# Performance work log

Hardware: AMD Instinct MI355X
Metric: run time of the kernel (lower is better)

The kernel has to match this reference:

```python
import jax, jax.numpy as jnp
from jax import lax
import numpy as np

D_MODEL, D_STATE, D_CONV, EXPAND = 512, 16, 4, 2
D_INNER = EXPAND * D_MODEL
B_SZ, SEQ = 16, 2048


def setup_inputs() -> dict:
    key = jax.random.key(0)
    ks = jax.random.split(key, 8)
    s = 0.02
    x = jax.random.normal(ks[0], (B_SZ, SEQ, D_MODEL), jnp.float32)
    W_in = jax.random.normal(ks[1], (2 * D_INNER, D_MODEL), jnp.float32) * s
    conv_w = jax.random.normal(ks[2], (D_INNER, 1, D_CONV), jnp.float32) * s
    conv_b = jnp.zeros((D_INNER,), jnp.float32)
    W_x = jax.random.normal(ks[3], (2 * D_STATE, D_INNER), jnp.float32) * s
    W_dt = jax.random.normal(ks[4], (D_INNER, D_INNER), jnp.float32) * s
    b_dt = jnp.zeros((D_INNER,), jnp.float32)
    # A_log = -logspace(log10(0.001), log10(1.0), d_state), exactly as in source
    A_log = jnp.asarray(-np.logspace(np.log10(0.001), 0.0, D_STATE), jnp.float32)
    D = jnp.ones((D_INNER,), jnp.float32) * 0.1
    W_out = jax.random.normal(ks[5], (D_MODEL, D_INNER), jnp.float32) * s
    ln_g = jnp.ones((D_MODEL,), jnp.float32)
    ln_b = jnp.zeros((D_MODEL,), jnp.float32)
    return dict(x=x, W_in=W_in, conv_w=conv_w, conv_b=conv_b, W_x=W_x,
                W_dt=W_dt, b_dt=b_dt, A_log=A_log, D=D, W_out=W_out,
                ln_g=ln_g, ln_b=ln_b)


def _selective_scan(u, delta, A, B, C, Dp):
    # u, delta: [b, s, di]; B, C: [b, s, ds]; A: [ds]; Dp: [di]
    def step(state, inp):
        d_t, u_t, B_t, C_t = inp            # [b,di],[b,di],[b,ds],[b,ds]
        dA = jnp.exp(jnp.clip(d_t[:, :, None] * A[None, None, :], -5.0, 5.0))
        dBu = (d_t * u_t)[:, :, None] * B_t[:, None, :]
        state = dA * state + dBu            # [b,di,ds]
        y_t = jnp.einsum('bds,bs->bd', state, C_t)
        return state, y_t

    b = u.shape[0]
    init = jnp.zeros((b, D_INNER, D_STATE), u.dtype)
    xs = (delta.transpose(1, 0, 2), u.transpose(1, 0, 2),
          B.transpose(1, 0, 2), C.transpose(1, 0, 2))
    _, ys = lax.scan(step, init, xs)        # [s, b, di]
    return ys.transpose(1, 0, 2) + u * Dp


def reference(x, W_in, conv_w, conv_b, W_x, W_dt, b_dt, A_log, D, W_out, ln_g, ln_b):
    x = jnp.clip(x, -10.0, 10.0)
    x_and_res = x @ W_in.T                  # [b, s, 2*di]
    x_p, res = jnp.split(x_and_res, 2, axis=-1)
    # causal depthwise conv1d (left pad d_conv-1, truncate to seq_len)
    xc = lax.conv_general_dilated(
        x_p.transpose(0, 2, 1), conv_w, window_strides=(1,),
        padding=[(D_CONV - 1, 0)], dimension_numbers=('NCH', 'OIH', 'NCH'),
        feature_group_count=D_INNER)
    xc = (xc + conv_b[None, :, None]).transpose(0, 2, 1)  # [b, s, di]
    xc = jax.nn.silu(xc)
    ssm = xc @ W_x.T                        # [b, s, 2*ds]
    Bm, Cm = jnp.split(ssm, 2, axis=-1)
    dt = xc @ W_dt.T + b_dt                 # [b, s, di]
    y = _selective_scan(xc, dt, A_log, Bm, Cm, D)
    y = y * jax.nn.silu(res)
    out = y @ W_out.T + x
    # LayerNorm (eps=1e-5)
    mu = out.mean(-1, keepdims=True)
    var = ((out - mu) ** 2).mean(-1, keepdims=True)
    return (out - mu) * lax.rsqrt(var + 1e-5) * ln_g + ln_b
```

## Files before the change

### kernel.cpp

```cpp
#include <hip/hip_runtime.h>
#include <hip/hip_bf16.h>
#include <math.h>

#define B_SZ 16
#define SEQ 2048
#define D_MODEL 512
#define D_INNER 1024
#define D_STATE 16
#define D_CONV 4
#define NSEG 32
#define SEGLEN (SEQ / NSEG)
#define GRP (SEGLEN / 4)
#define LOG2E 1.44269504f

typedef __attribute__((ext_vector_type(8))) short short8;
typedef __attribute__((ext_vector_type(4))) float f32x4;
typedef const __attribute__((address_space(1))) void* gas_ptr;
typedef __attribute__((address_space(3))) void* las_ptr;

__device__ __forceinline__ float bf2f(unsigned int bits16) {
    union { unsigned int i; float f; } v; v.i = bits16 << 16; return v.f;
}
__device__ __forceinline__ unsigned short f2bf(float f) {
    union { float f; unsigned int i; } v; v.f = f;
    unsigned int r = v.i + 0x7FFFu + ((v.i >> 16) & 1u);
    return (unsigned short)(r >> 16);
}
__device__ __forceinline__ void async_g2l(const void* g, void* l) {
    __builtin_amdgcn_global_load_lds((gas_ptr)g, (las_ptr)l, 16, 0, 0);
}
__device__ __forceinline__ float fast_exp2(float x) { return __builtin_amdgcn_exp2f(x); }
__device__ __forceinline__ float fast_rcp(float x)  { return __builtin_amdgcn_rcpf(x); }
__device__ __forceinline__ float clamp3(float x, float lo, float hi) {
    return __builtin_amdgcn_fmed3f(x, lo, hi);
}
__device__ __forceinline__ float silu(float x) {
    return x * fast_rcp(1.f + fast_exp2(-x * LOG2E));
}
__device__ __forceinline__ void vm_wait0() { asm volatile("s_waitcnt vmcnt(0)" ::: "memory"); }
__device__ __forceinline__ void vm_wait3() { asm volatile("s_waitcnt vmcnt(3)" ::: "memory"); }
__device__ __forceinline__ void vm_wait4() { asm volatile("s_waitcnt vmcnt(4)" ::: "memory"); }

__global__ __launch_bounds__(256) void cast_bf16(
    const float4* __restrict__ in, ushort4* __restrict__ out, int n4, int do_clip)
{
    int i = blockIdx.x * 256 + threadIdx.x;
    if (i >= n4) return;
    float4 v = in[i];
    if (do_clip) {
        v.x = clamp3(v.x, -10.f, 10.f);
        v.y = clamp3(v.y, -10.f, 10.f);
        v.z = clamp3(v.z, -10.f, 10.f);
        v.w = clamp3(v.w, -10.f, 10.f);
    }
    ushort4 o;
    o.x = f2bf(v.x); o.y = f2bf(v.y); o.z = f2bf(v.z); o.w = f2bf(v.w);
    out[i] = o;
}

__global__ __launch_bounds__(256) void cast5(
    const float4* __restrict__ W_in, const float4* __restrict__ W_dt,
    const float4* __restrict__ W_out, const float4* __restrict__ W_x,
    const float4* __restrict__ x,
    ushort4* __restrict__ Wib, ushort4* __restrict__ Wdtb,
    ushort4* __restrict__ Wob, ushort4* __restrict__ Wxb,
    ushort4* __restrict__ xbf, int n4x)
{
    const int A0 = 262144;
    const int A1 = A0 + 262144;
    const int A2 = A1 + 131072;
    const int A3 = A2 + 8192;
    int i = blockIdx.x * 256 + threadIdx.x;
    const float4* src; ushort4* dst; int j; int clip = 0;
    if (i < A0)      { src = W_in;  dst = Wib;  j = i; }
    else if (i < A1) { src = W_dt;  dst = Wdtb; j = i - A0; }
    else if (i < A2) { src = W_out; dst = Wob;  j = i - A1; }
    else if (i < A3) { src = W_x;   dst = Wxb;  j = i - A2; }
    else             { j = i - A3; if (j >= n4x) return; src = x; dst = xbf; clip = 1; }
    float4 v = src[j];
    if (clip) {
        v.x = clamp3(v.x, -10.f, 10.f);
        v.y = clamp3(v.y, -10.f, 10.f);
        v.z = clamp3(v.z, -10.f, 10.f);
        v.w = clamp3(v.w, -10.f, 10.f);
    }
    ushort4 o;
    o.x = f2bf(v.x); o.y = f2bf(v.y); o.z = f2bf(v.z); o.w = f2bf(v.w);
    dst[j] = o;
}

__global__ __launch_bounds__(512, 4) void gemm_big(
    const unsigned short* __restrict__ A, const unsigned short* __restrict__ Bw,
    void* __restrict__ C, int K, int ldc, int nbn_shift,
    const float* __restrict__ bias,
    const float* __restrict__ add, int ldadd, int clip_add, int out_bf16)
{
    __shared__ unsigned short As[3][256][32];
    __shared__ unsigned short Bs[3][128][32];
    const int h = blockIdx.x;
    const int xk = h & 7;
    const int qb = h >> 3;
    const int bn = (qb & ((1 << nbn_shift) - 1)) * 128;
    const int bm = ((qb >> nbn_shift) * 8 + xk) * 256;
    const int tid = threadIdx.x;
    const int wv = tid >> 6;
    const int l  = tid & 63;
    const int lr = l >> 2;
    const int lc = l & 3;
    const int wm = (wv >> 1) * 64;
    const int wn = (wv & 1) * 64;
    const int r16 = l & 15;
    const int q   = l >> 4;
    const int gsw = (lc - ((lr >> 1) & 3)) & 3;
    const int ssw = ((q + ((r16 >> 1) & 3)) & 3) * 8;

    f32x4 acc[4][4];
    #pragma unroll
    for (int i = 0; i < 4; i++)
        #pragma unroll
        for (int j = 0; j < 4; j++)
            acc[i][j] = (f32x4){0.f, 0.f, 0.f, 0.f};

#define STAGEB(kk, bb) { \
        const int k0_ = (kk) * 32; \
        _Pragma("unroll") \
        for (int p_ = 0; p_ < 2; p_++) { \
            const int arow_ = wv * 32 + p_ * 16 + lr; \
            async_g2l((const char*)A + (((size_t)(bm + arow_)) * K + k0_ + gsw * 8) * 2, \
                      (char*)&As[bb][wv * 32 + p_ * 16][0]); \
        } \
        const int brow_ = wv * 16 + lr; \
        async_g2l((const char*)Bw + (((size_t)(bn + brow_)) * K + k0_ + gsw * 8) * 2, \
                  (char*)&Bs[bb][wv * 16][0]); \
    }

    const int nk = K >> 5;
    STAGEB(0, 0);
    STAGEB(1, 1);
    int c0 = 0, c1 = 1, c2 = 2;

    for (int kk = 0; kk < nk; kk++) {
        if (kk + 1 < nk) vm_wait3(); else vm_wait0();
        __builtin_amdgcn_s_barrier();

        short8 af[4], bfv[4];
        #pragma unroll
        for (int i = 0; i < 4; i++) {
            af[i]  = *(const short8*)&As[c0][wm + i * 16 + r16][ssw];
            bfv[i] = *(const short8*)&Bs[c0][wn + i * 16 + r16][ssw];
        }
        if (kk + 2 < nk) STAGEB(kk + 2, c2);

        #pragma unroll
        for (int i = 0; i < 4; i++)
            #pragma unroll
            for (int j = 0; j < 4; j++)
                acc[i][j] = __builtin_amdgcn_mfma_f32_16x16x32_bf16(
                    af[i], bfv[j], acc[i][j], 0, 0, 0);

        int t = c0; c0 = c1; c1 = c2; c2 = t;
    }
#undef STAGEB

    #pragma unroll
    for (int i = 0; i < 4; i++) {
        #pragma unroll
        for (int rr = 0; rr < 4; rr++) {
            int m = bm + wm + i * 16 + q * 4 + rr;
            #pragma unroll
            for (int j = 0; j < 4; j++) {
                int n = bn + wn + j * 16 + r16;
                float v = acc[i][j][rr];
                if (bias) v += bias[n];
                if (add) {
                    float a = add[(size_t)m * ldadd + n];
                    if (clip_add) a = clamp3(a, -10.f, 10.f);
                    v += a;
                }
                if (out_bf16)
                    ((unsigned short*)C)[(size_t)m * ldc + n] = f2bf(v);
                else
                    ((float*)C)[(size_t)m * ldc + n] = v;
            }
        }
    }
}

__global__ __launch_bounds__(256) void gemm_bf16(
    const unsigned short* __restrict__ A, const unsigned short* __restrict__ Bw,
    void* __restrict__ C, int K, int ldc, int nbn_shift,
    const float* __restrict__ bias,
    const float* __restrict__ add, int ldadd, int clip_add, int out_bf16)
{
    __shared__ unsigned short As[3][128][32];
    __shared__ unsigned short Bs[3][128][32];
    const int h = blockIdx.x;
    const int xk = h & 7;
    const int qb = h >> 3;
    const int bn = (qb & ((1 << nbn_shift) - 1)) * 128;
    const int bm = ((qb >> nbn_shift) * 8 + xk) * 128;
    const int tid = threadIdx.x;
    const int wv = tid >> 6;
    const int l  = tid & 63;
    const int lr = l >> 2;
    const int lc = l & 3;
    const int wm = (wv >> 1) * 64;
    const int wn = (wv & 1) * 64;
    const int r16 = l & 15;
    const int q   = l >> 4;
    const int gsw = (lc - ((lr >> 1) & 3)) & 3;
    const int ssw = ((q + ((r16 >> 1) & 3)) & 3) * 8;

    f32x4 acc[4][4];
    #pragma unroll
    for (int i = 0; i < 4; i++)
        #pragma unroll
        for (int j = 0; j < 4; j++)
            acc[i][j] = (f32x4){0.f, 0.f, 0.f, 0.f};

#define STAGE(kk, bb) { \
        const int k0_ = (kk) * 32; \
        _Pragma("unroll") \
        for (int p_ = 0; p_ < 2; p_++) { \
            const int row_ = wv * 32 + p_ * 16 + lr; \
            async_g2l((const char*)A + (((size_t)(bm + row_)) * K + k0_ + gsw * 8) * 2, \
                      (char*)&As[bb][wv * 32 + p_ * 16][0]); \
            async_g2l((const char*)Bw + (((size_t)(bn + row_)) * K + k0_ + gsw * 8) * 2, \
                      (char*)&Bs[bb][wv * 32 + p_ * 16][0]); \
        } }

    const int nk = K >> 5;
    STAGE(0, 0);
    STAGE(1, 1);
    int c0 = 0, c1 = 1, c2 = 2;

    for (int kk = 0; kk < nk; kk++) {
        if (kk + 1 < nk) vm_wait4(); else vm_wait0();
        __builtin_amdgcn_s_barrier();

        short8 af[4], bfv[4];
        #pragma unroll
        for (int i = 0; i < 4; i++) {
            af[i]  = *(const short8*)&As[c0][wm + i * 16 + r16][ssw];
            bfv[i] = *(const short8*)&Bs[c0][wn + i * 16 + r16][ssw];
        }
        if (kk + 2 < nk) STAGE(kk + 2, c2);

        #pragma unroll
        for (int i = 0; i < 4; i++)
            #pragma unroll
            for (int j = 0; j < 4; j++)
                acc[i][j] = __builtin_amdgcn_mfma_f32_16x16x32_bf16(
                    af[i], bfv[j], acc[i][j], 0, 0, 0);

        int t = c0; c0 = c1; c1 = c2; c2 = t;
    }
#undef STAGE

    #pragma unroll
    for (int i = 0; i < 4; i++) {
        #pragma unroll
        for (int rr = 0; rr < 4; rr++) {
            int m = bm + wm + i * 16 + q * 4 + rr;
            #pragma unroll
            for (int j = 0; j < 4; j++) {
                int n = bn + wn + j * 16 + r16;
                float v = acc[i][j][rr];
                if (bias) v += bias[n];
                if (add) {
                    float a = add[(size_t)m * ldadd + n];
                    if (clip_add) a = clamp3(a, -10.f, 10.f);
                    v += a;
                }
                if (out_bf16)
                    ((unsigned short*)C)[(size_t)m * ldc + n] = f2bf(v);
                else
                    ((float*)C)[(size_t)m * ldc + n] = v;
            }
        }
    }
}

__global__ __launch_bounds__(256) void gemm_bc(
    const unsigned short* __restrict__ A, const unsigned short* __restrict__ Bw,
    float* __restrict__ C)
{
    const int tid = threadIdx.x;
    const int wv  = tid >> 6;
    const int l   = tid & 63;
    const int r16 = l & 15;
    const int q   = l >> 4;
    const int row0 = blockIdx.x * 64 + wv * 16;

    const unsigned short* ap  = A  + (size_t)(row0 + r16) * 1024 + q * 8;
    const unsigned short* bp0 = Bw + (size_t)r16 * 1024 + q * 8;
    const unsigned short* bp1 = Bw + (size_t)(16 + r16) * 1024 + q * 8;

    f32x4 acc0 = {0.f, 0.f, 0.f, 0.f}, acc1 = {0.f, 0.f, 0.f, 0.f};
    #pragma unroll 4
    for (int k = 0; k < 1024; k += 32) {
        short8 af = *(const short8*)(ap + k);
        short8 b0 = *(const short8*)(bp0 + k);
        short8 b1 = *(const short8*)(bp1 + k);
        acc0 = __builtin_amdgcn_mfma_f32_16x16x32_bf16(af, b0, acc0, 0, 0, 0);
        acc1 = __builtin_amdgcn_mfma_f32_16x16x32_bf16(af, b1, acc1, 0, 0, 0);
    }
    #pragma unroll
    for (int rr = 0; rr < 4; rr++) {
        int m = row0 + q * 4 + rr;
        C[(size_t)m * 32 + r16]      = acc0[rr];
        C[(size_t)m * 32 + 16 + r16] = acc1[rr];
    }
}

__global__ __launch_bounds__(256) void conv_silu(
    const unsigned short* __restrict__ xp, const float* __restrict__ cw,
    const float* __restrict__ cb, unsigned short* __restrict__ xc)
{
    int idx = blockIdx.x * 256 + threadIdx.x;
    int c4 = (idx & 255) << 2;
    int bt = idx >> 8;
    int t  = bt & (SEQ - 1);

    float4 acc = *(const float4*)(cb + c4);
    float4 w0 = *(const float4*)(cw + (c4 + 0) * 4);
    float4 w1 = *(const float4*)(cw + (c4 + 1) * 4);
    float4 w2 = *(const float4*)(cw + (c4 + 2) * 4);
    float4 w3 = *(const float4*)(cw + (c4 + 3) * 4);

    #pragma unroll
    for (int k = 0; k < D_CONV; k++) {
        int tt = t - (D_CONV - 1) + k;
        if (tt >= 0) {
            ushort4 xv = *(const ushort4*)(xp + (size_t)(bt - (D_CONV - 1) + k) * 2048 + c4);
            acc.x += bf2f(xv.x) * ((const float*)&w0)[k];
            acc.y += bf2f(xv.y) * ((const float*)&w1)[k];
            acc.z += bf2f(xv.z) * ((const float*)&w2)[k];
            acc.w += bf2f(xv.w) * ((const float*)&w3)[k];
        }
    }
    ushort4 o;
    o.x = f2bf(silu(acc.x));
    o.y = f2bf(silu(acc.y));
    o.z = f2bf(silu(acc.z));
    o.w = f2bf(silu(acc.w));
    *(ushort4*)(xc + (size_t)bt * 1024 + c4) = o;
}

__global__ __launch_bounds__(128, 4) void scan_phaseA(
    const unsigned short* __restrict__ xpres, const float* __restrict__ BC,
    const unsigned short* __restrict__ xc, const float* __restrict__ A_log,
    float* __restrict__ stA, float* __restrict__ prA)
{
    __shared__ float bc_lds[SEGLEN][32];
    const int bx = blockIdx.x;
    const int seg = bx & (NSEG - 1);
    const int dg  = (bx >> 5) & 15;
    const int b   = bx >> 9;
    if (seg == NSEG - 1) return;
    const int tid  = threadIdx.x;
    const int wv   = tid >> 6;
    const int half = (tid >> 5) & 1;
    const int dl   = tid & 31;
    const int d    = dg * 64 + wv * 32 + dl;
    const int n0   = half * 8;

    const size_t rowbase = (size_t)b * SEQ + (size_t)seg * SEGLEN;
    const float* BCp = BC + rowbase * 32;

    #pragma unroll
    for (int c = 0; c < 4; c++)
        async_g2l(BCp + c * 512 + tid * 4,
                  (char*)&bc_lds[0][0] + c * 2048 + tid * 16);

    float A2[8];
    #pragma unroll
    for (int n = 0; n < 8; n++) A2[n] = A_log[n0 + n] * LOG2E;

    const unsigned short* dtp = xpres + rowbase * 2048 + d;
    const unsigned short* up  = xc + rowbase * 1024 + d;

    float st[8] = {};
    float se[8] = {};
    unsigned short dta[4], dtb[4], ua[4], ub[4];

#define LOADGA(g, dt_, u_) { \
        _Pragma("unroll") for (int jj = 0; jj < 4; ++jj) { \
            const int t_ = (g) * 4 + jj; \
            dt_[jj] = dtp[(size_t)t_ * 2048]; \
            u_[jj]  = up[(size_t)t_ * 1024]; \
        } }

#define COMPGA(g, dt_, u_) { \
        _Pragma("unroll") for (int jj = 0; jj < 4; ++jj) { \
            const int t_ = (g) * 4 + jj; \
            const float dtv_ = bf2f(dt_[jj]); \
            const float du_ = dtv_ * bf2f(u_[jj]); \
            float Bv_[8]; \
            *(float4*)&Bv_[0] = *(const float4*)&bc_lds[t_][n0]; \
            *(float4*)&Bv_[4] = *(const float4*)&bc_lds[t_][n0 + 4]; \
            _Pragma("unroll") for (int n = 0; n < 8; ++n) { \
                const float e_ = dtv_ * A2[n]; \
                se[n] += e_; \
                st[n] = fast_exp2(e_) * st[n] + du_ * Bv_[n]; \
            } } }

    LOADGA(0, dta, ua);
    __syncthreads();

    for (int g = 0; g < GRP; g += 2) {
        LOADGA(g + 1, dtb, ub);
        COMPGA(g, dta, ua);
        if (g + 2 < GRP) LOADGA(g + 2, dta, ua);
        COMPGA(g + 1, dtb, ub);
    }
#undef LOADGA
#undef COMPGA

    size_t o = ((size_t)b * NSEG + seg) * 16384 + (size_t)half * 8192 + (size_t)d * 4;
    *(float4*)(stA + o)        = *(float4*)&st[0];
    *(float4*)(stA + o + 4096) = *(float4*)&st[4];
    float4 p0, p1;
    p0.x = fast_exp2(clamp3(se[0], -115.41f, 115.41f));
    p0.y = fast_exp2(clamp3(se[1], -115.41f, 115.41f));
    p0.z = fast_exp2(clamp3(se[2], -115.41f, 115.41f));
    p0.w = fast_exp2(clamp3(se[3], -115.41f, 115.41f));
    p1.x = fast_exp2(clamp3(se[4], -115.41f, 115.41f));
    p1.y = fast_exp2(clamp3(se[5], -115.41f, 115.41f));
    p1.z = fast_exp2(clamp3(se[6], -115.41f, 115.41f));
    p1.w = fast_exp2(clamp3(se[7], -115.41f, 115.41f));
    *(float4*)(prA + o)        = p0;
    *(float4*)(prA + o + 4096) = p1;
}

__global__ __launch_bounds__(256) void scan_combine(
    float* __restrict__ stA, const float* __restrict__ prA, int total)
{
    int idx = blockIdx.x * 256 + threadIdx.x;
    if (idx >= total) return;
    int dn = idx & 16383;
    int b  = idx >> 14;
    float prev = 0.f;
    #pragma unroll 4
    for (int s = 0; s < NSEG; s++) {
        size_t o = ((size_t)b * NSEG + s) * 16384 + dn;
        float a = stA[o], pr = prA[o];
        stA[o] = prev;
        prev = a + pr * prev;
    }
}

__global__ __launch_bounds__(128, 4) void scan_phaseC(
    const unsigned short* __restrict__ xpres, const float* __restrict__ BC,
    const unsigned short* __restrict__ xc, const float* __restrict__ A_log,
    const float* __restrict__ Dvec, const float* __restrict__ stIn,
    unsigned short* __restrict__ y_bf)
{
    __shared__ float bc_lds[SEGLEN][32];
    const int bx = blockIdx.x;
    const int seg = bx & (NSEG - 1);
    const int dg  = (bx >> 5) & 15;
    const int b   = bx >> 9;
    const int tid  = threadIdx.x;
    const int wv   = tid >> 6;
    const int half = (tid >> 5) & 1;
    const int dl   = tid & 31;
    const int d    = dg * 64 + wv * 32 + dl;
    const int n0   = half * 8;

    const size_t rowbase = (size_t)b * SEQ + (size_t)seg * SEGLEN;
    const float* BCp = BC + rowbase * 32;

    #pragma unroll
    for (int c = 0; c < 4; c++)
        async_g2l(BCp + c * 512 + tid * 4,
                  (char*)&bc_lds[0][0] + c * 2048 + tid * 16);

    float A2[8];
    #pragma unroll
    for (int n = 0; n < 8; n++) A2[n] = A_log[n0 + n] * LOG2E;
    const float Dp = Dvec[d];

    const unsigned short* dtp  = xpres + rowbase * 2048 + d;
    const unsigned short* resp = xpres + rowbase * 2048 + 1024 + d;
    const unsigned short* up   = xc + rowbase * 1024 + d;
    unsigned short* yp = y_bf + rowbase * 1024 + d;

    float st[8];
    size_t o = ((size_t)b * NSEG + seg) * 16384 + (size_t)half * 8192 + (size_t)d * 4;
    *(float4*)&st[0] = *(const float4*)(stIn + o);
    *(float4*)&st[4] = *(const float4*)(stIn + o + 4096);

    unsigned short dta[4], dtb[4], ua[4], ub[4], ra[4], rb[4];

#define LOADGC(g, dt_, r_, u_) { \
        _Pragma("unroll") for (int jj = 0; jj < 4; ++jj) { \
            const int t_ = (g) * 4 + jj; \
            dt_[jj] = dtp[(size_t)t_ * 2048]; \
            r_[jj]  = resp[(size_t)t_ * 2048]; \
            u_[jj]  = up[(size_t)t_ * 1024]; \
        } }

#define COMPGC(g, dt_, r_, u_) { \
        _Pragma("unroll") for (int jj = 0; jj < 4; ++jj) { \
            const int t_ = (g) * 4 + jj; \
            const float dtv_ = bf2f(dt_[jj]); \
            const float uu_ = bf2f(u_[jj]); \
            const float du_ = dtv_ * uu_; \
            float V_[8]; \
            *(float4*)&V_[0] = *(const float4*)&bc_lds[t_][n0]; \
            *(float4*)&V_[4] = *(const float4*)&bc_lds[t_][n0 + 4]; \
            _Pragma("unroll") for (int n = 0; n < 8; ++n) { \
                const float e_ = dtv_ * A2[n]; \
                st[n] = fast_exp2(e_) * st[n] + du_ * V_[n]; \
            } \
            *(float4*)&V_[0] = *(const float4*)&bc_lds[t_][16 + n0]; \
            *(float4*)&V_[4] = *(const float4*)&bc_lds[t_][16 + n0 + 4]; \
            float y_ = 0.f; \
            _Pragma("unroll") for (int n = 0; n < 8; ++n) \
                y_ += st[n] * V_[n]; \
            y_ += __shfl_xor(y_, 32); \
            if (half == 0) { \
                const float outv_ = (y_ + uu_ * Dp) * silu(bf2f(r_[jj])); \
                yp[(size_t)t_ * 1024] = f2bf(outv_); \
            } } }

    LOADGC(0, dta, ra, ua);
    __syncthreads();

    for (int g = 0; g < GRP; g += 2) {
        LOADGC(g + 1, dtb, rb, ub);
        COMPGC(g, dta, ra, ua);
        if (g + 2 < GRP) LOADGC(g + 2, dta, ra, ua);
        COMPGC(g + 1, dtb, rb, ub);
    }
#undef LOADGC
#undef COMPGC
}

__global__ __launch_bounds__(128) void ln_kernel(
    float* __restrict__ out, const float* __restrict__ g,
    const float* __restrict__ bta)
{
    const int row = blockIdx.x;
    float* p = out + (size_t)row * D_MODEL;
    const int tid = threadIdx.x;

    float4 v = ((const float4*)p)[tid];
    float s1 = v.x + v.y + v.z + v.w;
    float s2 = v.x * v.x + v.y * v.y + v.z * v.z + v.w * v.w;
    #pragma unroll
    for (int off = 32; off > 0; off >>= 1) {
        s1 += __shfl_xor(s1, off);
        s2 += __shfl_xor(s2, off);
    }
    __shared__ float r1[2], r2[2];
    if ((tid & 63) == 0) { r1[tid >> 6] = s1; r2[tid >> 6] = s2; }
    __syncthreads();
    s1 = r1[0] + r1[1];
    s2 = r2[0] + r2[1];

    const float mu  = s1 * (1.f / D_MODEL);
    const float var = s2 * (1.f / D_MODEL) - mu * mu;
    const float rstd = rsqrtf(var + 1e-5f);

    float4 gg = ((const float4*)g)[tid];
    float4 bb = ((const float4*)bta)[tid];
    float4 o;
    o.x = (v.x - mu) * rstd * gg.x + bb.x;
    o.y = (v.y - mu) * rstd * gg.y + bb.y;
    o.z = (v.z - mu) * rstd * gg.z + bb.z;
    o.w = (v.w - mu) * rstd * gg.w + bb.w;
    ((float4*)p)[tid] = o;
}

extern "C" void kernel_launch(void* const* d_in, const int* in_sizes, int n_in,
                              void* d_out, int out_size, void* d_ws, size_t ws_size,
                              hipStream_t stream)
{
    const float* x      = (const float*)d_in[0];
    const float* W_in   = (const float*)d_in[1];
    const float* conv_w = (const float*)d_in[2];
    const float* conv_b = (const float*)d_in[3];
    const float* W_x    = (const float*)d_in[4];
    const float* W_dt   = (const float*)d_in[5];
    const float* b_dt   = (const float*)d_in[6];
    const float* A_log  = (const float*)d_in[7];
    const float* Dv     = (const float*)d_in[8];
    const float* W_out  = (const float*)d_in[9];
    const float* ln_g   = (const float*)d_in[10];
    const float* ln_b   = (const float*)d_in[11];
    float* out = (float*)d_out;

    const size_t szWin  = (size_t)2048 * 512;
    const size_t szWdt  = (size_t)1024 * 1024;
    const size_t szWout = (size_t)512 * 1024;
    const size_t szWx   = (size_t)32 * 1024;
    char* p = (char*)d_ws;
    unsigned short* Wib  = (unsigned short*)p; p += szWin * 2;
    unsigned short* Wdtb = (unsigned short*)p; p += szWdt * 2;
    unsigned short* Wob  = (unsigned short*)p; p += szWout * 2;
    unsigned short* Wxb  = (unsigned short*)p; p += szWx * 2;
    const size_t fixed_bytes = (size_t)(p - (char*)d_ws);

    const size_t per_batch =
        (size_t)SEQ * 2048 * 2
      + (size_t)SEQ * 1024 * 2
      + (size_t)SEQ * 1024 * 2
      + (size_t)SEQ * 32 * 4
      + (size_t)2 * NSEG * 1024 * 16 * 4;
    int cb = 16;
    while (cb > 1 && fixed_bytes + (size_t)cb * per_batch > ws_size) cb >>= 1;
    const int Mc = cb * SEQ;

    unsigned short* xpres = (unsigned short*)p; p += (size_t)Mc * 2048 * 2;
    unsigned short* ybuf  = (unsigned short*)p; p += (size_t)Mc * 1024 * 2;
    unsigned short* x_bf  = ybuf;
    unsigned short* xc_bf = (unsigned short*)p; p += (size_t)Mc * 1024 * 2;
    float*          BCb   = (float*)p;          p += (size_t)Mc * 32 * 4;
    float*          stA   = (float*)p;          p += (size_t)cb * NSEG * 16384 * 4;
    float*          prA   = (float*)p;

    const int n4x0 = Mc * 128;
    cast5<<<(663552 + n4x0 + 255) / 256, 256, 0, stream>>>(
        (const float4*)W_in, (const float4*)W_dt, (const float4*)W_out,
        (const float4*)W_x, (const float4*)x,
        (ushort4*)Wib, (ushort4*)Wdtb, (ushort4*)Wob, (ushort4*)Wxb,
        (ushort4*)x_bf, n4x0);

    for (int b0 = 0; b0 < B_SZ; b0 += cb) {
        const float* xk   = x   + (size_t)b0 * SEQ * D_MODEL;
        float*       outk = out + (size_t)b0 * SEQ * D_MODEL;

        if (b0 > 0)
            cast_bf16<<<(Mc * 512 / 4) / 256, 256, 0, stream>>>(
                (const float4*)xk, (ushort4*)x_bf, Mc * 512 / 4, 1);

        gemm_big<<<16 * (Mc / 256), 512, 0, stream>>>(
            x_bf, Wib, xpres, 512, 2048, 4, nullptr, nullptr, 0, 0, 1);

        conv_silu<<<Mc, 256, 0, stream>>>(xpres, conv_w, conv_b, xc_bf);

        gemm_bc<<<Mc / 64, 256, 0, stream>>>(xc_bf, Wxb, BCb);

        gemm_big<<<8 * (Mc / 256), 512, 0, stream>>>(
            xc_bf, Wdtb, xpres, 1024, 2048, 3, b_dt, nullptr, 0, 0, 1);

        scan_phaseA<<<cb * NSEG * 16, 128, 0, stream>>>(xpres, BCb, xc_bf, A_log, stA, prA);
        scan_combine<<<(cb * 16384 + 255) / 256, 256, 0, stream>>>(stA, prA, cb * 16384);
        scan_phaseC<<<cb * NSEG * 16, 128, 0, stream>>>(xpres, BCb, xc_bf, A_log, Dv, stA, ybuf);

        gemm_bf16<<<4 * (Mc / 128), 256, 0, stream>>>(
            ybuf, Wob, outk, 1024, 512, 2, nullptr, xk, 512, 1, 0);

        ln_kernel<<<Mc, 128, 0, stream>>>(outk, ln_g, ln_b);
    }
}
```

Measured before the change: 842.8 us.

## Store per-segment dt sums instead of decay products and reuse xpres for y

Phase A now writes one summed dt per channel and segment instead of 16 precomputed decay products. The combine kernel rebuilds each decay as exp2(A*sum_dt), which removes the prA buffer and its traffic. The scan output y is written in place into the dt half of xpres, which is no longer needed at that point. The GEMMs gain an lda parameter so they can read this strided layout, and x_bf now aliases stA. Together this shrinks the workspace, so larger batch chunks may fit, at the cost of strided A-operand loads in the output GEMM.

```diff
diff --git a/kernel.cpp b/kernel.cpp
--- a/kernel.cpp
+++ b/kernel.cpp
@@ -91,7 +91,7 @@
 
 __global__ __launch_bounds__(512, 4) void gemm_big(
     const unsigned short* __restrict__ A, const unsigned short* __restrict__ Bw,
-    void* __restrict__ C, int K, int ldc, int nbn_shift,
+    void* __restrict__ C, int K, int lda, int ldc, int nbn_shift,
     const float* __restrict__ bias,
     const float* __restrict__ add, int ldadd, int clip_add, int out_bf16)
 {
@@ -126,7 +126,7 @@
         _Pragma("unroll") \
         for (int p_ = 0; p_ < 2; p_++) { \
             const int arow_ = wv * 32 + p_ * 16 + lr; \
-            async_g2l((const char*)A + (((size_t)(bm + arow_)) * K + k0_ + gsw * 8) * 2, \
+            async_g2l((const char*)A + (((size_t)(bm + arow_)) * lda + k0_ + gsw * 8) * 2, \
                       (char*)&As[bb][wv * 32 + p_ * 16][0]); \
         } \
         const int brow_ = wv * 16 + lr; \
@@ -188,7 +188,7 @@
 
 __global__ __launch_bounds__(256) void gemm_bf16(
     const unsigned short* __restrict__ A, const unsigned short* __restrict__ Bw,
-    void* __restrict__ C, int K, int ldc, int nbn_shift,
+    void* __restrict__ C, int K, int lda, int ldc, int nbn_shift,
     const float* __restrict__ bias,
     const float* __restrict__ add, int ldadd, int clip_add, int out_bf16)
 {
@@ -223,7 +223,7 @@
         _Pragma("unroll") \
         for (int p_ = 0; p_ < 2; p_++) { \
             const int row_ = wv * 32 + p_ * 16 + lr; \
-            async_g2l((const char*)A + (((size_t)(bm + row_)) * K + k0_ + gsw * 8) * 2, \
+            async_g2l((const char*)A + (((size_t)(bm + row_)) * lda + k0_ + gsw * 8) * 2, \
                       (char*)&As[bb][wv * 32 + p_ * 16][0]); \
             async_g2l((const char*)Bw + (((size_t)(bn + row_)) * K + k0_ + gsw * 8) * 2, \
                       (char*)&Bs[bb][wv * 32 + p_ * 16][0]); \
@@ -350,7 +350,7 @@
 __global__ __launch_bounds__(128, 4) void scan_phaseA(
     const unsigned short* __restrict__ xpres, const float* __restrict__ BC,
     const unsigned short* __restrict__ xc, const float* __restrict__ A_log,
-    float* __restrict__ stA, float* __restrict__ prA)
+    float* __restrict__ stA, float* __restrict__ sdt)
 {
     __shared__ float bc_lds[SEGLEN][32];
     const int bx = blockIdx.x;
@@ -381,7 +381,7 @@
     const unsigned short* up  = xc + rowbase * 1024 + d;
 
     float st[8] = {};
-    float se[8] = {};
+    float sdtv = 0.f;
     unsigned short dta[4], dtb[4], ua[4], ub[4];
 
 #define LOADGA(g, dt_, u_) { \
@@ -396,12 +396,12 @@
             const int t_ = (g) * 4 + jj; \
             const float dtv_ = bf2f(dt_[jj]); \
             const float du_ = dtv_ * bf2f(u_[jj]); \
+            sdtv += dtv_; \
             float Bv_[8]; \
             *(float4*)&Bv_[0] = *(const float4*)&bc_lds[t_][n0]; \
             *(float4*)&Bv_[4] = *(const float4*)&bc_lds[t_][n0 + 4]; \
             _Pragma("unroll") for (int n = 0; n < 8; ++n) { \
                 const float e_ = dtv_ * A2[n]; \
-                se[n] += e_; \
                 st[n] = fast_exp2(e_) * st[n] + du_ * Bv_[n]; \
             } } }
 
@@ -420,41 +420,39 @@
     size_t o = ((size_t)b * NSEG + seg) * 16384 + (size_t)half * 8192 + (size_t)d * 4;
     *(float4*)(stA + o)        = *(float4*)&st[0];
     *(float4*)(stA + o + 4096) = *(float4*)&st[4];
-    float4 p0, p1;
-    p0.x = fast_exp2(clamp3(se[0], -115.41f, 115.41f));
-    p0.y = fast_exp2(clamp3(se[1], -115.41f, 115.41f));
-    p0.z = fast_exp2(clamp3(se[2], -115.41f, 115.41f));
-    p0.w = fast_exp2(clamp3(se[3], -115.41f, 115.41f));
-    p1.x = fast_exp2(clamp3(se[4], -115.41f, 115.41f));
-    p1.y = fast_exp2(clamp3(se[5], -115.41f, 115.41f));
-    p1.z = fast_exp2(clamp3(se[6], -115.41f, 115.41f));
-    p1.w = fast_exp2(clamp3(se[7], -115.41f, 115.41f));
-    *(float4*)(prA + o)        = p0;
-    *(float4*)(prA + o + 4096) = p1;
+    if (half == 0)
+        sdt[((size_t)b * NSEG + seg) * 1024 + d] = sdtv;
 }
 
 __global__ __launch_bounds__(256) void scan_combine(
-    float* __restrict__ stA, const float* __restrict__ prA, int total)
+    float* __restrict__ stA, const float* __restrict__ sdt,
+    const float* __restrict__ A_log, int total)
 {
     int idx = blockIdx.x * 256 + threadIdx.x;
     if (idx >= total) return;
-    int dn = idx & 16383;
-    int b  = idx >> 14;
+    int pos = idx & 16383;
+    int b   = idx >> 14;
+    const int half = pos >> 13;
+    const int k    = (pos >> 12) & 1;
+    const int d    = (pos >> 2) & 1023;
+    const int j    = pos & 3;
+    const float A2n = A_log[half * 8 + k * 4 + j] * LOG2E;
     float prev = 0.f;
     #pragma unroll 4
     for (int s = 0; s < NSEG; s++) {
-        size_t o = ((size_t)b * NSEG + s) * 16384 + dn;
-        float a = stA[o], pr = prA[o];
+        size_t o = ((size_t)b * NSEG + s) * 16384 + pos;
+        float a = stA[o];
+        float pr = fast_exp2(clamp3(A2n * sdt[((size_t)b * NSEG + s) * 1024 + d],
+                                    -115.41f, 115.41f));
         stA[o] = prev;
         prev = a + pr * prev;
     }
 }
 
 __global__ __launch_bounds__(128, 4) void scan_phaseC(
-    const unsigned short* __restrict__ xpres, const float* __restrict__ BC,
+    unsigned short* __restrict__ xpres, const float* __restrict__ BC,
     const unsigned short* __restrict__ xc, const float* __restrict__ A_log,
-    const float* __restrict__ Dvec, const float* __restrict__ stIn,
-    unsigned short* __restrict__ y_bf)
+    const float* __restrict__ Dvec, const float* __restrict__ stIn)
 {
     __shared__ float bc_lds[SEGLEN][32];
     const int bx = blockIdx.x;
@@ -484,7 +482,7 @@
     const unsigned short* dtp  = xpres + rowbase * 2048 + d;
     const unsigned short* resp = xpres + rowbase * 2048 + 1024 + d;
     const unsigned short* up   = xc + rowbase * 1024 + d;
-    unsigned short* yp = y_bf + rowbase * 1024 + d;
+    unsigned short* yp = xpres + rowbase * 2048 + d;
 
     float st[8];
     size_t o = ((size_t)b * NSEG + seg) * 16384 + (size_t)half * 8192 + (size_t)d * 4;
@@ -522,7 +520,7 @@
             y_ += __shfl_xor(y_, 32); \
             if (half == 0) { \
                 const float outv_ = (y_ + uu_ * Dp) * silu(bf2f(r_[jj])); \
-                yp[(size_t)t_ * 1024] = f2bf(outv_); \
+                yp[(size_t)t_ * 2048] = f2bf(outv_); \
             } } }
 
     LOADGC(0, dta, ra, ua);
@@ -606,20 +604,19 @@
     const size_t per_batch =
         (size_t)SEQ * 2048 * 2
       + (size_t)SEQ * 1024 * 2
-      + (size_t)SEQ * 1024 * 2
       + (size_t)SEQ * 32 * 4
-      + (size_t)2 * NSEG * 1024 * 16 * 4;
+      + (size_t)NSEG * 16384 * 4
+      + (size_t)NSEG * 1024 * 4;
     int cb = 16;
     while (cb > 1 && fixed_bytes + (size_t)cb * per_batch > ws_size) cb >>= 1;
     const int Mc = cb * SEQ;
 
     unsigned short* xpres = (unsigned short*)p; p += (size_t)Mc * 2048 * 2;
-    unsigned short* ybuf  = (unsigned short*)p; p += (size_t)Mc * 1024 * 2;
-    unsigned short* x_bf  = ybuf;
     unsigned short* xc_bf = (unsigned short*)p; p += (size_t)Mc * 1024 * 2;
     float*          BCb   = (float*)p;          p += (size_t)Mc * 32 * 4;
     float*          stA   = (float*)p;          p += (size_t)cb * NSEG * 16384 * 4;
-    float*          prA   = (float*)p;
+    float*          sdt   = (float*)p;
+    unsigned short* x_bf  = (unsigned short*)stA;
 
     const int n4x0 = Mc * 128;
     cast5<<<(663552 + n4x0 + 255) / 256, 256, 0, stream>>>(
@@ -637,21 +634,21 @@
                 (const float4*)xk, (ushort4*)x_bf, Mc * 512 / 4, 1);
 
         gemm_big<<<16 * (Mc / 256), 512, 0, stream>>>(
-            x_bf, Wib, xpres, 512, 2048, 4, nullptr, nullptr, 0, 0, 1);
+            x_bf, Wib, xpres, 512, 512, 2048, 4, nullptr, nullptr, 0, 0, 1);
 
         conv_silu<<<Mc, 256, 0, stream>>>(xpres, conv_w, conv_b, xc_bf);
 
         gemm_bc<<<Mc / 64, 256, 0, stream>>>(xc_bf, Wxb, BCb);
 
         gemm_big<<<8 * (Mc / 256), 512, 0, stream>>>(
-            xc_bf, Wdtb, xpres, 1024, 2048, 3, b_dt, nullptr, 0, 0, 1);
-
-        scan_phaseA<<<cb * NSEG * 16, 128, 0, stream>>>(xpres, BCb, xc_bf, A_log, stA, prA);
-        scan_combine<<<(cb * 16384 + 255) / 256, 256, 0, stream>>>(stA, prA, cb * 16384);
-        scan_phaseC<<<cb * NSEG * 16, 128, 0, stream>>>(xpres, BCb, xc_bf, A_log, Dv, stA, ybuf);
+            xc_bf, Wdtb, xpres, 1024, 1024, 2048, 3, b_dt, nullptr, 0, 0, 1);
+
+        scan_phaseA<<<cb * NSEG * 16, 128, 0, stream>>>(xpres, BCb, xc_bf, A_log, stA, sdt);
+        scan_combine<<<(cb * 16384 + 255) / 256, 256, 0, stream>>>(stA, sdt, A_log, cb * 16384);
+        scan_phaseC<<<cb * NSEG * 16, 128, 0, stream>>>(xpres, BCb, xc_bf, A_log, Dv, stA);
 
         gemm_bf16<<<4 * (Mc / 128), 256, 0, stream>>>(
-            ybuf, Wob, outk, 1024, 512, 2, nullptr, xk, 512, 1, 0);
+            xpres, Wob, outk, 1024, 2048, 512, 2, nullptr, xk, 512, 1, 0);
 
         ln_kernel<<<Mc, 128, 0, stream>>>(outk, ln_g, ln_b);
     }
```

New measurement: 788.7 us. 1.07x faster.
